# Optimization experiments

Hardware: AMD Instinct MI355X
Metric: run time of the kernel (lower is better)

Reference implementation:

```python
import jax, jax.numpy as jnp
import numpy as np

B, H, W = 8, 64, 64
D_MODEL, D_STATE, D_INNER, DT_RANK, K = 96, 16, 192, 6, 4
EPS = 1e-6


def setup_inputs() -> dict:
    key = jax.random.key(0)
    ks = jax.random.split(key, 9)
    f = lambda k, s, sc=0.02: jax.random.normal(k, s, dtype=jnp.float32) * sc
    return {
        "x": jax.random.normal(ks[0], (B, H, W, D_MODEL), jnp.float32),
        "in_proj_w": f(ks[1], (2 * D_INNER, D_MODEL)),
        "conv_w": f(ks[2], (D_INNER, 1, 3, 3), 0.1),
        "conv_b": jnp.zeros((D_INNER,), jnp.float32),
        "x_proj_w": f(ks[3], (K * (DT_RANK + 2 * D_STATE), D_INNER)),
        "dt_projs_w": f(ks[4], (K * D_INNER, DT_RANK), 0.1),
        "A_logs": jnp.log(jax.random.uniform(ks[5], (K * D_INNER, D_STATE), jnp.float32, 1.0, 16.0)),
        "Ds": jnp.ones((K * D_INNER,), jnp.float32),
        "dt_projs_bias": f(ks[6], (K * D_INNER,), 0.5),
        "norm_w": jnp.ones((D_INNER,), jnp.float32),
        "norm_b": jnp.zeros((D_INNER,), jnp.float32),
        "out_proj_w": f(ks[7], (D_MODEL, D_INNER)),
    }


def _ss2d(x, in_proj_w, conv_w, conv_b, x_proj_w, dt_projs_w, A_logs, Ds,
          dt_projs_bias, norm_w, norm_b, out_proj_w):
    silu = jax.nn.silu
    Bb, Hh, Ww, _ = x.shape
    L = Hh * Ww
    # in_proj, split x/z, z gate activation
    xz = x @ in_proj_w.T                                   # (B,H,W,2*Di)
    xx, z = jnp.split(xz, 2, axis=-1)
    z = silu(z)
    # depthwise conv 3x3 in NCHW
    xc = jnp.transpose(xx, (0, 3, 1, 2))                   # (B,Di,H,W)
    xc = jax.lax.conv_general_dilated(
        xc, conv_w, (1, 1), ((1, 1), (1, 1)),
        dimension_numbers=("NCHW", "OIHW", "NCHW"),
        feature_group_count=D_INNER) + conv_b[None, :, None, None]
    xc = silu(xc)
    # 4-way cross scan: hw, wh (transposed), and their reversals
    x_hw = xc.reshape(Bb, D_INNER, L)
    x_wh = jnp.transpose(xc, (0, 1, 3, 2)).reshape(Bb, D_INNER, L)
    xs = jnp.stack([x_hw, x_wh, x_hw[..., ::-1], x_wh[..., ::-1]], axis=1)  # (B,K,Di,L)
    # per-group projections for dt, B, C
    xpw = x_proj_w.reshape(K, DT_RANK + 2 * D_STATE, D_INNER)
    x_dbl = jnp.einsum("bkdl,kcd->bkcl", xs, xpw)
    dts, Bs, Cs = jnp.split(x_dbl, [DT_RANK, DT_RANK + D_STATE], axis=2)
    dtw = dt_projs_w.reshape(K, D_INNER, DT_RANK)
    dts = jnp.einsum("bkrl,kdr->bkdl", dts, dtw)           # (B,K,Di,L)
    A = -jnp.exp(A_logs).reshape(K, D_INNER, D_STATE)      # (K,Di,N)
    dt = jax.nn.softplus(dts + dt_projs_bias.reshape(1, K, D_INNER, 1))
    # selective scan over L
    def step(h, inp):
        u_t, dt_t, B_t, C_t = inp                          # (B,K,Di),(B,K,Di),(B,K,N),(B,K,N)
        dA = jnp.exp(dt_t[..., None] * A)                  # (B,K,Di,N)
        h = h * dA + (dt_t * u_t)[..., None] * B_t[:, :, None, :]
        y = jnp.einsum("bkdn,bkn->bkd", h, C_t)
        return h, y
    h0 = jnp.zeros((Bb, K, D_INNER, D_STATE), jnp.float32)
    seq = (jnp.moveaxis(xs, -1, 0), jnp.moveaxis(dt, -1, 0),
           jnp.moveaxis(Bs, -1, 0), jnp.moveaxis(Cs, -1, 0))
    _, ysL = jax.lax.scan(step, h0, seq)
    ys = jnp.moveaxis(ysL, 0, -1)                          # (B,K,Di,L)
    ys = ys + xs * Ds.reshape(1, K, D_INNER, 1)
    # cross merge: invert flips and wh-transpose, then sum the 4 directions
    y = ys[:, 0] + ys[:, 2][..., ::-1]
    yw = ys[:, 1] + ys[:, 3][..., ::-1]
    y = y + yw.reshape(Bb, D_INNER, Ww, Hh).transpose(0, 1, 3, 2).reshape(Bb, D_INNER, L)
    y = y.reshape(Bb, D_INNER, Hh, Ww).transpose(0, 2, 3, 1)   # (B,H,W,Di)
    # out LayerNorm over channels
    mean = y.mean(-1, keepdims=True)
    var = ((y - mean) ** 2).mean(-1, keepdims=True)
    y = (y - mean) / jnp.sqrt(var + EPS) * norm_w + norm_b
    # gate and out_proj
    y = y * z
    return y @ out_proj_w.T                                # (B,H,W,d_model)


def reference(x, in_proj_w, conv_w, conv_b, x_proj_w, dt_projs_w, A_logs, Ds,
              dt_projs_bias, norm_w, norm_b, out_proj_w):
    return _ss2d(x, in_proj_w, conv_w, conv_b, x_proj_w, dt_projs_w, A_logs, Ds,
                 dt_projs_bias, norm_w, norm_b, out_proj_w)
```

## Files before the change

kernel.cpp:

```cpp
#include <hip/hip_runtime.h>
#include <hip/hip_bf16.h>
#include <math.h>

#define BB 8
#define HS 64
#define WS 64
#define LL 4096
#define DM 96
#define DI 192
#define NS 16
#define RR 6
#define KK 4
#define NCH 64
#define LC 64
#define XP 16
#define EPSN 1e-6f

typedef __attribute__((ext_vector_type(2))) float f32x2;

__device__ __forceinline__ float fsilu(float x) { return x / (1.f + __expf(-x)); }
__device__ __forceinline__ float rexp2(float x) {
    float r; asm("v_exp_f32 %0, %1" : "=v"(r) : "v"(x)); return r;
}
__device__ __forceinline__ float rlog2(float x) {
    float r; asm("v_log_f32 %0, %1" : "=v"(r) : "v"(x)); return r;
}
__device__ __forceinline__ f32x2 pk_mul(f32x2 a, f32x2 b) {
    f32x2 d; asm("v_pk_mul_f32 %0, %1, %2" : "=v"(d) : "v"(a), "v"(b)); return d;
}
__device__ __forceinline__ f32x2 pk_fma(f32x2 a, f32x2 b, f32x2 c) {
    f32x2 d; asm("v_pk_fma_f32 %0, %1, %2, %3" : "=v"(d) : "v"(a), "v"(b), "v"(c)); return d;
}
__device__ __forceinline__ float fsoftplus(float x) {
    float t = rexp2(x * 1.44269504f);
    float r = 0.69314718f * rlog2(1.f + t);
    return (x > 20.f) ? x : r;
}
__device__ __forceinline__ int lmap(int k, int t) {
    int tt = (k >= 2) ? (LL - 1 - t) : t;
    if (k & 1) tt = ((tt & 63) << 6) | (tt >> 6);
    return tt;
}

__global__ __launch_bounds__(192) void k_inproj(const float* __restrict__ x,
        const float* __restrict__ Win, float* __restrict__ xx, float* __restrict__ zs) {
    __shared__ __align__(16) float xrow[32][96];
    int p0 = blockIdx.x * 32;
    int tid = threadIdx.x;
    {
        const float4* src = (const float4*)(x + (size_t)p0 * 96);
        float4* dst = (float4*)&xrow[0][0];
        #pragma unroll
        for (int e = 0; e < 4; ++e) dst[tid + e * 192] = src[tid + e * 192];
    }
    __syncthreads();
    int c = tid % 96;
    int pg = tid / 96;
    const float4* w0 = (const float4*)(Win + (size_t)c * 96);
    const float4* w1 = (const float4*)(Win + (size_t)(c + 96) * 96);
    const float4* w2 = (const float4*)(Win + (size_t)(c + 192) * 96);
    const float4* w3 = (const float4*)(Win + (size_t)(c + 288) * 96);
    float a0v[16], a1v[16], a2v[16], a3v[16];
    #pragma unroll
    for (int p = 0; p < 16; ++p) { a0v[p] = 0.f; a1v[p] = 0.f; a2v[p] = 0.f; a3v[p] = 0.f; }
    for (int i = 0; i < 24; ++i) {
        float4 q0 = w0[i], q1 = w1[i], q2 = w2[i], q3 = w3[i];
        #pragma unroll
        for (int p = 0; p < 16; ++p) {
            float4 x4 = *(const float4*)&xrow[pg * 16 + p][i * 4];
            a0v[p] += q0.x * x4.x + q0.y * x4.y + q0.z * x4.z + q0.w * x4.w;
            a1v[p] += q1.x * x4.x + q1.y * x4.y + q1.z * x4.z + q1.w * x4.w;
            a2v[p] += q2.x * x4.x + q2.y * x4.y + q2.z * x4.z + q2.w * x4.w;
            a3v[p] += q3.x * x4.x + q3.y * x4.y + q3.z * x4.z + q3.w * x4.w;
        }
    }
    #pragma unroll
    for (int p = 0; p < 16; ++p) {
        size_t row = (size_t)(p0 + pg * 16 + p) * DI;
        xx[row + c]      = a0v[p];
        xx[row + c + 96] = a1v[p];
        zs[row + c]      = fsilu(a2v[p]);
        zs[row + c + 96] = fsilu(a3v[p]);
    }
}

__global__ __launch_bounds__(256) void k_conv(const float* __restrict__ xx,
        const float* __restrict__ cw, const float* __restrict__ cb,
        float* __restrict__ xc) {
    int idx = blockIdx.x * 256 + threadIdx.x;
    int d = idx % DI; int P = idx / DI;
    int l = P & (LL - 1); int h = l >> 6; int w = l & 63;
    float acc = cb[d];
    #pragma unroll
    for (int i = 0; i < 3; ++i) {
        int hh = h + i - 1;
        if ((unsigned)hh < 64u) {
            #pragma unroll
            for (int j = 0; j < 3; ++j) {
                int ww = w + j - 1;
                if ((unsigned)ww < 64u)
                    acc += xx[(size_t)(P + (i - 1) * 64 + (j - 1)) * DI + d] * cw[d * 9 + i * 3 + j];
            }
        }
    }
    xc[idx] = fsilu(acc);
}

__global__ __launch_bounds__(192) void k_xdbl(const float* __restrict__ xc,
        const float* __restrict__ xpw, float* __restrict__ dts_raw,
        float* __restrict__ Bs, float* __restrict__ Cs) {
    __shared__ __align__(16) float xt[XP][DI];
    int tid = threadIdx.x;
    int p0 = blockIdx.x * XP;
    {
        const float4* src = (const float4*)(xc + (size_t)p0 * DI);
        float4* dst = (float4*)&xt[0][0];
        #pragma unroll
        for (int e = 0; e < XP * DI / 4 / 192; ++e) dst[tid + e * 192] = src[tid + e * 192];
    }
    __syncthreads();
    int c = tid;
    int k = c / 38, c2 = c % 38;
    const float4* w4p = (const float4*)(xpw + (size_t)c * DI);
    float acc[XP];
    #pragma unroll
    for (int p = 0; p < XP; ++p) acc[p] = 0.f;
    if (c < 152) {
        #pragma unroll 4
        for (int i = 0; i < DI / 4; ++i) {
            float4 w4 = w4p[i];
            #pragma unroll
            for (int p = 0; p < XP; ++p) {
                float4 x4 = *(const float4*)&xt[p][i * 4];
                acc[p] += w4.x * x4.x + w4.y * x4.y + w4.z * x4.z + w4.w * x4.w;
            }
        }
        #pragma unroll
        for (int p = 0; p < XP; ++p) {
            int P = p0 + p;
            int b = P >> 12; int l = P & (LL - 1);
            int lt = ((l & 63) << 6) | (l >> 6);
            int tk = (k == 0) ? l : (k == 1) ? lt : (k == 2) ? (LL - 1 - l) : (LL - 1 - lt);
            size_t it = ((size_t)(b * KK + k) * LL + tk);
            if (c2 < RR)            dts_raw[it * RR + c2] = acc[p];
            else if (c2 < RR + NS)  Bs[it * NS + (c2 - RR)] = acc[p];
            else                    Cs[it * NS + (c2 - RR - NS)] = acc[p];
        }
    }
}

__global__ __launch_bounds__(192) void k_scan1(const float* __restrict__ xc,
        const float* __restrict__ dts_raw, const float* __restrict__ Bsg,
        const float* __restrict__ A_logs, const float* __restrict__ dtw,
        const float* __restrict__ dtb,
        float* __restrict__ asum_g, float* __restrict__ hpart) {
    __shared__ __align__(16) float dts_s[LC * 8];
    __shared__ __align__(16) float bs_s[LC * NS];
    int bi = blockIdx.x;
    int b = bi >> 8; int rem = bi & 255; int k = rem >> 6; int c0 = rem & 63;
    int t0 = c0 * LC;
    int d = threadIdx.x;
    size_t g0 = (size_t)(b * KK + k) * LL + t0;
    for (int e = d; e < LC * RR; e += DI) dts_s[(e / RR) * 8 + (e % RR)] = dts_raw[g0 * RR + e];
    for (int e = d; e < LC * NS; e += DI) bs_s[e] = Bsg[g0 * NS + e];
    __syncthreads();
    int kd = k * DI + d;
    f32x2 Ar2v[8];
    #pragma unroll
    for (int n2 = 0; n2 < 8; ++n2) {
        Ar2v[n2].x = -__expf(A_logs[(size_t)kd * NS + 2 * n2]) * 1.44269504f;
        Ar2v[n2].y = -__expf(A_logs[(size_t)kd * NS + 2 * n2 + 1]) * 1.44269504f;
    }
    f32x2 dw2[3];
    #pragma unroll
    for (int r = 0; r < 3; ++r) { dw2[r].x = dtw[kd * RR + 2 * r]; dw2[r].y = dtw[kd * RR + 2 * r + 1]; }
    float bias = dtb[kd];
    f32x2 h2[8];
    #pragma unroll
    for (int n2 = 0; n2 < 8; ++n2) h2[n2] = (f32x2){0.f, 0.f};
    float asum = 0.f;
    const float* xcb = xc + (size_t)b * LL * DI + d;
    float uu[4];
    #pragma unroll
    for (int j = 0; j < 4; ++j) uu[j] = xcb[(size_t)lmap(k, t0 + j) * DI];
    for (int tg = 0; tg < LC; tg += 4) {
        float un[4];
        int tb = t0 + ((tg + 4 < LC) ? (tg + 4) : tg);
        #pragma unroll
        for (int j = 0; j < 4; ++j) un[j] = xcb[(size_t)lmap(k, tb + j) * DI];
        #pragma unroll
        for (int j = 0; j < 4; ++j) {
            int t = tg + j;
            float4 q4 = *(const float4*)&dts_s[t * 8];
            float2 q2 = *(const float2*)&dts_s[t * 8 + 4];
            f32x2 a2 = pk_mul((f32x2){q4.x, q4.y}, dw2[0]);
            a2 = pk_fma((f32x2){q4.z, q4.w}, dw2[1], a2);
            a2 = pk_fma((f32x2){q2.x, q2.y}, dw2[2], a2);
            float dt = fsoftplus(bias + a2.x + a2.y);
            asum += dt;
            float dtu = dt * uu[j];
            f32x2 dt2 = {dt, dt}, dtu2 = {dtu, dtu};
            #pragma unroll
            for (int n4 = 0; n4 < 4; ++n4) {
                float4 b4 = *(const float4*)&bs_s[t * NS + n4 * 4];
                f32x2 tl = pk_mul(dt2, Ar2v[n4 * 2]);
                f32x2 th = pk_mul(dt2, Ar2v[n4 * 2 + 1]);
                f32x2 el = {rexp2(tl.x), rexp2(tl.y)};
                f32x2 eh = {rexp2(th.x), rexp2(th.y)};
                h2[n4 * 2]     = pk_fma(h2[n4 * 2],     el, pk_mul(dtu2, (f32x2){b4.x, b4.y}));
                h2[n4 * 2 + 1] = pk_fma(h2[n4 * 2 + 1], eh, pk_mul(dtu2, (f32x2){b4.z, b4.w}));
            }
        }
        #pragma unroll
        for (int j = 0; j < 4; ++j) uu[j] = un[j];
    }
    asum_g[(size_t)bi * DI + d] = asum;
    size_t base = ((size_t)bi * DI + d) * NS;
    #pragma unroll
    for (int n4 = 0; n4 < 4; ++n4) {
        float4 hv = make_float4(h2[n4 * 2].x, h2[n4 * 2].y, h2[n4 * 2 + 1].x, h2[n4 * 2 + 1].y);
        *(float4*)&hpart[base + n4 * 4] = hv;
    }
}

__global__ __launch_bounds__(256) void k_mid(const float* __restrict__ asum_g,
        const float* __restrict__ A_logs, float* __restrict__ hpp) {
    int g = blockIdx.x * 256 + threadIdx.x;
    int bk = g / (DI * NS);
    int rem = g % (DI * NS);
    int d = rem >> 4; int n = rem & 15;
    int k = bk & 3;
    float Ar2 = -__expf(A_logs[(size_t)(k * DI + d) * NS + n]) * 1.44269504f;
    float h = 0.f;
    for (int c = 0; c < NCH; ++c) {
        size_t row = (size_t)(bk * NCH + c) * DI + d;
        float a = rexp2(Ar2 * asum_g[row]);
        size_t ix = row * NS + n;
        float hp = hpp[ix];
        hpp[ix] = h;
        h = a * h + hp;
    }
}

__global__ __launch_bounds__(192) void k_scan2(const float* __restrict__ xc,
        const float* __restrict__ dts_raw, const float* __restrict__ Bsg,
        const float* __restrict__ Csg, const float* __restrict__ A_logs,
        const float* __restrict__ dtw, const float* __restrict__ dtb,
        const float* __restrict__ hinb, float* __restrict__ ysb) {
    __shared__ __align__(16) float dts_s[LC * 8];
    __shared__ __align__(16) float bs_s[LC * NS];
    __shared__ __align__(16) float cs_s[LC * NS];
    int bi = blockIdx.x;
    int b = bi >> 8; int rem = bi & 255; int k = rem >> 6; int c0 = rem & 63;
    int t0 = c0 * LC;
    int d = threadIdx.x;
    size_t g0 = (size_t)(b * KK + k) * LL + t0;
    for (int e = d; e < LC * RR; e += DI) dts_s[(e / RR) * 8 + (e % RR)] = dts_raw[g0 * RR + e];
    for (int e = d; e < LC * NS; e += DI) bs_s[e] = Bsg[g0 * NS + e];
    for (int e = d; e < LC * NS; e += DI) cs_s[e] = Csg[g0 * NS + e];
    __syncthreads();
    int kd = k * DI + d;
    f32x2 Ar2v[8];
    #pragma unroll
    for (int n2 = 0; n2 < 8; ++n2) {
        Ar2v[n2].x = -__expf(A_logs[(size_t)kd * NS + 2 * n2]) * 1.44269504f;
        Ar2v[n2].y = -__expf(A_logs[(size_t)kd * NS + 2 * n2 + 1]) * 1.44269504f;
    }
    f32x2 dw2[3];
    #pragma unroll
    for (int r = 0; r < 3; ++r) { dw2[r].x = dtw[kd * RR + 2 * r]; dw2[r].y = dtw[kd * RR + 2 * r + 1]; }
    float bias = dtb[kd];
    size_t base = ((size_t)bi * DI + d) * NS;
    f32x2 h2[8];
    #pragma unroll
    for (int n4 = 0; n4 < 4; ++n4) {
        float4 hv = *(const float4*)&hinb[base + n4 * 4];
        h2[n4 * 2]     = (f32x2){hv.x, hv.y};
        h2[n4 * 2 + 1] = (f32x2){hv.z, hv.w};
    }
    const float* xcb = xc + (size_t)b * LL * DI + d;
    float* ysw = ysb + g0 * DI + d;
    float uu[4];
    #pragma unroll
    for (int j = 0; j < 4; ++j) uu[j] = xcb[(size_t)lmap(k, t0 + j) * DI];
    for (int tg = 0; tg < LC; tg += 4) {
        float un[4];
        int tb = t0 + ((tg + 4 < LC) ? (tg + 4) : tg);
        #pragma unroll
        for (int j = 0; j < 4; ++j) un[j] = xcb[(size_t)lmap(k, tb + j) * DI];
        #pragma unroll
        for (int j = 0; j < 4; ++j) {
            int t = tg + j;
            float4 q4 = *(const float4*)&dts_s[t * 8];
            float2 q2 = *(const float2*)&dts_s[t * 8 + 4];
            f32x2 a2 = pk_mul((f32x2){q4.x, q4.y}, dw2[0]);
            a2 = pk_fma((f32x2){q4.z, q4.w}, dw2[1], a2);
            a2 = pk_fma((f32x2){q2.x, q2.y}, dw2[2], a2);
            float dt = fsoftplus(bias + a2.x + a2.y);
            float dtu = dt * uu[j];
            f32x2 dt2 = {dt, dt}, dtu2 = {dtu, dtu};
            f32x2 y2 = {0.f, 0.f};
            #pragma unroll
            for (int n4 = 0; n4 < 4; ++n4) {
                float4 b4 = *(const float4*)&bs_s[t * NS + n4 * 4];
                float4 c4 = *(const float4*)&cs_s[t * NS + n4 * 4];
                f32x2 tl = pk_mul(dt2, Ar2v[n4 * 2]);
                f32x2 th = pk_mul(dt2, Ar2v[n4 * 2 + 1]);
                f32x2 el = {rexp2(tl.x), rexp2(tl.y)};
                f32x2 eh = {rexp2(th.x), rexp2(th.y)};
                h2[n4 * 2]     = pk_fma(h2[n4 * 2],     el, pk_mul(dtu2, (f32x2){b4.x, b4.y}));
                h2[n4 * 2 + 1] = pk_fma(h2[n4 * 2 + 1], eh, pk_mul(dtu2, (f32x2){b4.z, b4.w}));
                y2 = pk_fma(h2[n4 * 2],     (f32x2){c4.x, c4.y}, y2);
                y2 = pk_fma(h2[n4 * 2 + 1], (f32x2){c4.z, c4.w}, y2);
            }
            ysw[(size_t)t * DI] = y2.x + y2.y;
        }
        #pragma unroll
        for (int j = 0; j < 4; ++j) uu[j] = un[j];
    }
}

__global__ __launch_bounds__(256) void k_final(const float* __restrict__ xc,
        const float* __restrict__ ysb, const float* __restrict__ Ds,
        const float* __restrict__ zs, const float* __restrict__ nw,
        const float* __restrict__ nb, const float* __restrict__ Wout,
        float* __restrict__ out) {
    __shared__ __align__(16) float gs[32][DI];
    int tid = threadIdx.x;
    int wv = tid >> 6, lane = tid & 63;
    int Pbase = blockIdx.x * 32;
    float nwv[3], nbv[3], sdv[3];
    #pragma unroll
    for (int j = 0; j < 3; ++j) {
        int c = lane + 64 * j;
        nwv[j] = nw[c]; nbv[j] = nb[c];
        sdv[j] = Ds[c] + Ds[DI + c] + Ds[2 * DI + c] + Ds[3 * DI + c];
    }
    for (int pi = 0; pi < 8; ++pi) {
        int pl = wv * 8 + pi;
        int P = Pbase + pl;
        int b = P >> 12, l = P & (LL - 1);
        size_t Poff = (size_t)P * DI;
        size_t r0 = ((size_t)(b * KK + 0) * LL + lmap(0, l)) * DI;
        size_t r1 = ((size_t)(b * KK + 1) * LL + lmap(1, l)) * DI;
        size_t r2 = ((size_t)(b * KK + 2) * LL + lmap(2, l)) * DI;
        size_t r3 = ((size_t)(b * KK + 3) * LL + lmap(3, l)) * DI;
        float v[3];
        #pragma unroll
        for (int j = 0; j < 3; ++j) {
            int c = lane + 64 * j;
            v[j] = xc[Poff + c] * sdv[j]
                 + ysb[r0 + c] + ysb[r1 + c] + ysb[r2 + c] + ysb[r3 + c];
        }
        float s = v[0] + v[1] + v[2];
        #pragma unroll
        for (int o = 32; o; o >>= 1) s += __shfl_xor(s, o);
        float mean = s * (1.f / 192.f);
        float ss = 0.f;
        #pragma unroll
        for (int j = 0; j < 3; ++j) { float dd = v[j] - mean; ss += dd * dd; }
        #pragma unroll
        for (int o = 32; o; o >>= 1) ss += __shfl_xor(ss, o);
        float rstd = rsqrtf(ss * (1.f / 192.f) + EPSN);
        #pragma unroll
        for (int j = 0; j < 3; ++j) {
            int c = lane + 64 * j;
            gs[pl][c] = ((v[j] - mean) * rstd * nwv[j] + nbv[j]) * zs[Poff + c];
        }
    }
    __syncthreads();
    int o = tid & 127;
    int pg = tid >> 7;
    if (o < DM) {
        const float* wr = Wout + (size_t)o * DI;
        float acc[16];
        #pragma unroll
        for (int p = 0; p < 16; ++p) acc[p] = 0.f;
        for (int k0 = 0; k0 < DI; k0 += 4) {
            float4 w4 = *(const float4*)(wr + k0);
            #pragma unroll
            for (int p = 0; p < 16; ++p) {
                float4 g4 = *(const float4*)(&gs[pg * 16 + p][k0]);
                acc[p] += w4.x * g4.x + w4.y * g4.y + w4.z * g4.z + w4.w * g4.w;
            }
        }
        #pragma unroll
        for (int p = 0; p < 16; ++p)
            out[(size_t)(Pbase + pg * 16 + p) * DM + o] = acc[p];
    }
}

extern "C" void kernel_launch(void* const* d_in, const int* in_sizes, int n_in,
                              void* d_out, int out_size, void* d_ws, size_t ws_size,
                              hipStream_t stream) {
    const float* x      = (const float*)d_in[0];
    const float* in_w   = (const float*)d_in[1];
    const float* conv_w = (const float*)d_in[2];
    const float* conv_b = (const float*)d_in[3];
    const float* xpw    = (const float*)d_in[4];
    const float* dtw    = (const float*)d_in[5];
    const float* A_logs = (const float*)d_in[6];
    const float* Ds     = (const float*)d_in[7];
    const float* dtb    = (const float*)d_in[8];
    const float* nw     = (const float*)d_in[9];
    const float* nb     = (const float*)d_in[10];
    const float* out_w  = (const float*)d_in[11];
    float* out = (float*)d_out;

    char* ws = (char*)d_ws;
    size_t off = 0;
    auto alloc = [&](size_t n) { float* p = (float*)(ws + off); off += n * sizeof(float); return p; };
    float* zs   = alloc((size_t)BB * LL * DI);
    float* xc   = alloc((size_t)BB * LL * DI);
    float* dts  = alloc((size_t)BB * KK * LL * RR);
    float* Bsb  = alloc((size_t)BB * KK * LL * NS);
    float* Csb  = alloc((size_t)BB * KK * LL * NS);
    float* asum = alloc((size_t)BB * KK * NCH * DI);
    float* hpp  = alloc((size_t)BB * KK * NCH * DI * NS);
    float* ysb  = alloc((size_t)BB * KK * LL * DI);
    float* xx   = ysb;

    k_inproj<<<BB * LL / 32, 192, 0, stream>>>(x, in_w, xx, zs);
    k_conv<<<BB * LL * DI / 256, 256, 0, stream>>>(xx, conv_w, conv_b, xc);
    k_xdbl<<<BB * LL / XP, 192, 0, stream>>>(xc, xpw, dts, Bsb, Csb);
    k_scan1<<<BB * KK * NCH, DI, 0, stream>>>(xc, dts, Bsb, A_logs, dtw, dtb, asum, hpp);
    k_mid<<<(BB * KK * DI * NS) / 256, 256, 0, stream>>>(asum, A_logs, hpp);
    k_scan2<<<BB * KK * NCH, DI, 0, stream>>>(xc, dts, Bsb, Csb, A_logs, dtw, dtb, hpp, ysb);
    k_final<<<BB * LL / 32, 256, 0, stream>>>(xc, ysb, Ds, zs, nw, nb, out_w, out);
}
```

Measured before the change: 426.2 us.

## Fuse chunked scan passes into single-pass decoupled look-back scan

Replaces the three-kernel chunked selective scan (local chunk scan, sequential carry kernel, rescan) with one kernel. Blocks take ordered tickets, publish chunk-local aggregates and inclusive prefixes with flags, then spin on predecessors using decoupled look-back to get their incoming state. This removes two kernel launches, the serial carry pass and the hpart/asum round trips between kernels. In exchange it adds spin-waiting, atomic traffic and a memset, and each block still runs the chunk recurrence twice.

```diff
diff --git a/kernel.cpp b/kernel.cpp
--- a/kernel.cpp
+++ b/kernel.cpp
@@ -13,6 +13,8 @@
 #define KK 4
 #define NCH 64
 #define LC 64
+#define NSTREAM (BB * KK)
+#define NBLK (NSTREAM * NCH)
 #define XP 16
 #define EPSN 1e-6f
 
@@ -40,6 +42,12 @@
     int tt = (k >= 2) ? (LL - 1 - t) : t;
     if (k & 1) tt = ((tt & 63) << 6) | (tt >> 6);
     return tt;
+}
+__device__ __forceinline__ float ald(const float* p) {
+    return __hip_atomic_load(p, __ATOMIC_RELAXED, __HIP_MEMORY_SCOPE_AGENT);
+}
+__device__ __forceinline__ void ast(float* p, float v) {
+    __hip_atomic_store(p, v, __ATOMIC_RELAXED, __HIP_MEMORY_SCOPE_AGENT);
 }
 
 __global__ __launch_bounds__(192) void k_inproj(const float* __restrict__ x,
@@ -149,111 +157,26 @@
     }
 }
 
-__global__ __launch_bounds__(192) void k_scan1(const float* __restrict__ xc,
-        const float* __restrict__ dts_raw, const float* __restrict__ Bsg,
-        const float* __restrict__ A_logs, const float* __restrict__ dtw,
-        const float* __restrict__ dtb,
-        float* __restrict__ asum_g, float* __restrict__ hpart) {
-    __shared__ __align__(16) float dts_s[LC * 8];
-    __shared__ __align__(16) float bs_s[LC * NS];
-    int bi = blockIdx.x;
-    int b = bi >> 8; int rem = bi & 255; int k = rem >> 6; int c0 = rem & 63;
-    int t0 = c0 * LC;
-    int d = threadIdx.x;
-    size_t g0 = (size_t)(b * KK + k) * LL + t0;
-    for (int e = d; e < LC * RR; e += DI) dts_s[(e / RR) * 8 + (e % RR)] = dts_raw[g0 * RR + e];
-    for (int e = d; e < LC * NS; e += DI) bs_s[e] = Bsg[g0 * NS + e];
-    __syncthreads();
-    int kd = k * DI + d;
-    f32x2 Ar2v[8];
-    #pragma unroll
-    for (int n2 = 0; n2 < 8; ++n2) {
-        Ar2v[n2].x = -__expf(A_logs[(size_t)kd * NS + 2 * n2]) * 1.44269504f;
-        Ar2v[n2].y = -__expf(A_logs[(size_t)kd * NS + 2 * n2 + 1]) * 1.44269504f;
-    }
-    f32x2 dw2[3];
-    #pragma unroll
-    for (int r = 0; r < 3; ++r) { dw2[r].x = dtw[kd * RR + 2 * r]; dw2[r].y = dtw[kd * RR + 2 * r + 1]; }
-    float bias = dtb[kd];
-    f32x2 h2[8];
-    #pragma unroll
-    for (int n2 = 0; n2 < 8; ++n2) h2[n2] = (f32x2){0.f, 0.f};
-    float asum = 0.f;
-    const float* xcb = xc + (size_t)b * LL * DI + d;
-    float uu[4];
-    #pragma unroll
-    for (int j = 0; j < 4; ++j) uu[j] = xcb[(size_t)lmap(k, t0 + j) * DI];
-    for (int tg = 0; tg < LC; tg += 4) {
-        float un[4];
-        int tb = t0 + ((tg + 4 < LC) ? (tg + 4) : tg);
-        #pragma unroll
-        for (int j = 0; j < 4; ++j) un[j] = xcb[(size_t)lmap(k, tb + j) * DI];
-        #pragma unroll
-        for (int j = 0; j < 4; ++j) {
-            int t = tg + j;
-            float4 q4 = *(const float4*)&dts_s[t * 8];
-            float2 q2 = *(const float2*)&dts_s[t * 8 + 4];
-            f32x2 a2 = pk_mul((f32x2){q4.x, q4.y}, dw2[0]);
-            a2 = pk_fma((f32x2){q4.z, q4.w}, dw2[1], a2);
-            a2 = pk_fma((f32x2){q2.x, q2.y}, dw2[2], a2);
-            float dt = fsoftplus(bias + a2.x + a2.y);
-            asum += dt;
-            float dtu = dt * uu[j];
-            f32x2 dt2 = {dt, dt}, dtu2 = {dtu, dtu};
-            #pragma unroll
-            for (int n4 = 0; n4 < 4; ++n4) {
-                float4 b4 = *(const float4*)&bs_s[t * NS + n4 * 4];
-                f32x2 tl = pk_mul(dt2, Ar2v[n4 * 2]);
-                f32x2 th = pk_mul(dt2, Ar2v[n4 * 2 + 1]);
-                f32x2 el = {rexp2(tl.x), rexp2(tl.y)};
-                f32x2 eh = {rexp2(th.x), rexp2(th.y)};
-                h2[n4 * 2]     = pk_fma(h2[n4 * 2],     el, pk_mul(dtu2, (f32x2){b4.x, b4.y}));
-                h2[n4 * 2 + 1] = pk_fma(h2[n4 * 2 + 1], eh, pk_mul(dtu2, (f32x2){b4.z, b4.w}));
-            }
-        }
-        #pragma unroll
-        for (int j = 0; j < 4; ++j) uu[j] = un[j];
-    }
-    asum_g[(size_t)bi * DI + d] = asum;
-    size_t base = ((size_t)bi * DI + d) * NS;
-    #pragma unroll
-    for (int n4 = 0; n4 < 4; ++n4) {
-        float4 hv = make_float4(h2[n4 * 2].x, h2[n4 * 2].y, h2[n4 * 2 + 1].x, h2[n4 * 2 + 1].y);
-        *(float4*)&hpart[base + n4 * 4] = hv;
-    }
-}
-
-__global__ __launch_bounds__(256) void k_mid(const float* __restrict__ asum_g,
-        const float* __restrict__ A_logs, float* __restrict__ hpp) {
-    int g = blockIdx.x * 256 + threadIdx.x;
-    int bk = g / (DI * NS);
-    int rem = g % (DI * NS);
-    int d = rem >> 4; int n = rem & 15;
-    int k = bk & 3;
-    float Ar2 = -__expf(A_logs[(size_t)(k * DI + d) * NS + n]) * 1.44269504f;
-    float h = 0.f;
-    for (int c = 0; c < NCH; ++c) {
-        size_t row = (size_t)(bk * NCH + c) * DI + d;
-        float a = rexp2(Ar2 * asum_g[row]);
-        size_t ix = row * NS + n;
-        float hp = hpp[ix];
-        hpp[ix] = h;
-        h = a * h + hp;
-    }
-}
-
-__global__ __launch_bounds__(192) void k_scan2(const float* __restrict__ xc,
+__global__ __launch_bounds__(192) void k_scan(const float* __restrict__ xc,
         const float* __restrict__ dts_raw, const float* __restrict__ Bsg,
         const float* __restrict__ Csg, const float* __restrict__ A_logs,
         const float* __restrict__ dtw, const float* __restrict__ dtb,
-        const float* __restrict__ hinb, float* __restrict__ ysb) {
+        int* __restrict__ flags, int* __restrict__ ticket,
+        float* __restrict__ asum_s, float* __restrict__ hpart_s,
+        float* __restrict__ hout_s, float* __restrict__ ysb) {
     __shared__ __align__(16) float dts_s[LC * 8];
     __shared__ __align__(16) float bs_s[LC * NS];
     __shared__ __align__(16) float cs_s[LC * NS];
-    int bi = blockIdx.x;
-    int b = bi >> 8; int rem = bi & 255; int k = rem >> 6; int c0 = rem & 63;
-    int t0 = c0 * LC;
+    __shared__ int s_tkt, s_flag;
     int d = threadIdx.x;
+    if (d == 0) s_tkt = atomicAdd(ticket, 1);
+    __syncthreads();
+    int tk = s_tkt;
+    int stream = tk % NSTREAM;
+    int c = tk / NSTREAM;
+    int b = stream >> 2, k = stream & 3;
+    int bi = stream * NCH + c;
+    int t0 = c * LC;
     size_t g0 = (size_t)(b * KK + k) * LL + t0;
     for (int e = d; e < LC * RR; e += DI) dts_s[(e / RR) * 8 + (e % RR)] = dts_raw[g0 * RR + e];
     for (int e = d; e < LC * NS; e += DI) bs_s[e] = Bsg[g0 * NS + e];
@@ -270,53 +193,150 @@
     #pragma unroll
     for (int r = 0; r < 3; ++r) { dw2[r].x = dtw[kd * RR + 2 * r]; dw2[r].y = dtw[kd * RR + 2 * r + 1]; }
     float bias = dtb[kd];
-    size_t base = ((size_t)bi * DI + d) * NS;
+    const float* xcb = xc + (size_t)b * LL * DI + d;
     f32x2 h2[8];
     #pragma unroll
-    for (int n4 = 0; n4 < 4; ++n4) {
-        float4 hv = *(const float4*)&hinb[base + n4 * 4];
-        h2[n4 * 2]     = (f32x2){hv.x, hv.y};
-        h2[n4 * 2 + 1] = (f32x2){hv.z, hv.w};
-    }
-    const float* xcb = xc + (size_t)b * LL * DI + d;
+    for (int n2 = 0; n2 < 8; ++n2) h2[n2] = (f32x2){0.f, 0.f};
+    float asum = 0.f;
+    {
+        float uu[4];
+        #pragma unroll
+        for (int j = 0; j < 4; ++j) uu[j] = xcb[(size_t)lmap(k, t0 + j) * DI];
+        for (int tg = 0; tg < LC; tg += 4) {
+            float un[4];
+            int tb = t0 + ((tg + 4 < LC) ? (tg + 4) : tg);
+            #pragma unroll
+            for (int j = 0; j < 4; ++j) un[j] = xcb[(size_t)lmap(k, tb + j) * DI];
+            #pragma unroll
+            for (int j = 0; j < 4; ++j) {
+                int t = tg + j;
+                float4 q4 = *(const float4*)&dts_s[t * 8];
+                float2 q2 = *(const float2*)&dts_s[t * 8 + 4];
+                f32x2 a2 = pk_mul((f32x2){q4.x, q4.y}, dw2[0]);
+                a2 = pk_fma((f32x2){q4.z, q4.w}, dw2[1], a2);
+                a2 = pk_fma((f32x2){q2.x, q2.y}, dw2[2], a2);
+                float dt = fsoftplus(bias + a2.x + a2.y);
+                asum += dt;
+                float dtu = dt * uu[j];
+                f32x2 dt2 = {dt, dt}, dtu2 = {dtu, dtu};
+                #pragma unroll
+                for (int n4 = 0; n4 < 4; ++n4) {
+                    float4 b4 = *(const float4*)&bs_s[t * NS + n4 * 4];
+                    f32x2 tl = pk_mul(dt2, Ar2v[n4 * 2]);
+                    f32x2 th = pk_mul(dt2, Ar2v[n4 * 2 + 1]);
+                    f32x2 el = {rexp2(tl.x), rexp2(tl.y)};
+                    f32x2 eh = {rexp2(th.x), rexp2(th.y)};
+                    h2[n4 * 2]     = pk_fma(h2[n4 * 2],     el, pk_mul(dtu2, (f32x2){b4.x, b4.y}));
+                    h2[n4 * 2 + 1] = pk_fma(h2[n4 * 2 + 1], eh, pk_mul(dtu2, (f32x2){b4.z, b4.w}));
+                }
+            }
+            #pragma unroll
+            for (int j = 0; j < 4; ++j) uu[j] = un[j];
+        }
+    }
+    size_t sb = (size_t)bi * DI + d;
+    size_t hb = sb * NS;
+    ast(&asum_s[sb], asum);
+    #pragma unroll
+    for (int n2 = 0; n2 < 8; ++n2) {
+        ast(&hpart_s[hb + 2 * n2], h2[n2].x);
+        ast(&hpart_s[hb + 2 * n2 + 1], h2[n2].y);
+    }
+    __threadfence();
+    __syncthreads();
+    if (c > 0 && d == 0)
+        __hip_atomic_store(&flags[bi], 1, __ATOMIC_RELEASE, __HIP_MEMORY_SCOPE_AGENT);
+    f32x2 hin[8], pA[8];
+    #pragma unroll
+    for (int n2 = 0; n2 < 8; ++n2) { hin[n2] = (f32x2){0.f, 0.f}; pA[n2] = (f32x2){1.f, 1.f}; }
+    if (c > 0) {
+        int j = c - 1;
+        while (true) {
+            __syncthreads();
+            if (d == 0) {
+                int f;
+                do { f = __hip_atomic_load(&flags[stream * NCH + j], __ATOMIC_ACQUIRE, __HIP_MEMORY_SCOPE_AGENT); } while (f == 0);
+                s_flag = f;
+            }
+            __syncthreads();
+            int f = s_flag;
+            size_t pb = ((size_t)(stream * NCH + j) * DI + d) * NS;
+            if (f == 2) {
+                #pragma unroll
+                for (int n2 = 0; n2 < 8; ++n2) {
+                    f32x2 hv = { ald(&hout_s[pb + 2 * n2]), ald(&hout_s[pb + 2 * n2 + 1]) };
+                    hin[n2] = pk_fma(pA[n2], hv, hin[n2]);
+                }
+                break;
+            } else {
+                #pragma unroll
+                for (int n2 = 0; n2 < 8; ++n2) {
+                    f32x2 hv = { ald(&hpart_s[pb + 2 * n2]), ald(&hpart_s[pb + 2 * n2 + 1]) };
+                    hin[n2] = pk_fma(pA[n2], hv, hin[n2]);
+                }
+                float aj = ald(&asum_s[(size_t)(stream * NCH + j) * DI + d]);
+                #pragma unroll
+                for (int n2 = 0; n2 < 8; ++n2) {
+                    f32x2 e = { rexp2(Ar2v[n2].x * aj), rexp2(Ar2v[n2].y * aj) };
+                    pA[n2] = pk_mul(pA[n2], e);
+                }
+                --j;
+            }
+        }
+    }
+    #pragma unroll
+    for (int n2 = 0; n2 < 8; ++n2) {
+        f32x2 e = { rexp2(Ar2v[n2].x * asum), rexp2(Ar2v[n2].y * asum) };
+        f32x2 ho = pk_fma(e, hin[n2], h2[n2]);
+        ast(&hout_s[hb + 2 * n2], ho.x);
+        ast(&hout_s[hb + 2 * n2 + 1], ho.y);
+    }
+    __threadfence();
+    __syncthreads();
+    if (d == 0)
+        __hip_atomic_store(&flags[bi], 2, __ATOMIC_RELEASE, __HIP_MEMORY_SCOPE_AGENT);
+    #pragma unroll
+    for (int n2 = 0; n2 < 8; ++n2) h2[n2] = hin[n2];
     float* ysw = ysb + g0 * DI + d;
-    float uu[4];
-    #pragma unroll
-    for (int j = 0; j < 4; ++j) uu[j] = xcb[(size_t)lmap(k, t0 + j) * DI];
-    for (int tg = 0; tg < LC; tg += 4) {
-        float un[4];
-        int tb = t0 + ((tg + 4 < LC) ? (tg + 4) : tg);
-        #pragma unroll
-        for (int j = 0; j < 4; ++j) un[j] = xcb[(size_t)lmap(k, tb + j) * DI];
-        #pragma unroll
-        for (int j = 0; j < 4; ++j) {
-            int t = tg + j;
-            float4 q4 = *(const float4*)&dts_s[t * 8];
-            float2 q2 = *(const float2*)&dts_s[t * 8 + 4];
-            f32x2 a2 = pk_mul((f32x2){q4.x, q4.y}, dw2[0]);
-            a2 = pk_fma((f32x2){q4.z, q4.w}, dw2[1], a2);
-            a2 = pk_fma((f32x2){q2.x, q2.y}, dw2[2], a2);
-            float dt = fsoftplus(bias + a2.x + a2.y);
-            float dtu = dt * uu[j];
-            f32x2 dt2 = {dt, dt}, dtu2 = {dtu, dtu};
-            f32x2 y2 = {0.f, 0.f};
-            #pragma unroll
-            for (int n4 = 0; n4 < 4; ++n4) {
-                float4 b4 = *(const float4*)&bs_s[t * NS + n4 * 4];
-                float4 c4 = *(const float4*)&cs_s[t * NS + n4 * 4];
-                f32x2 tl = pk_mul(dt2, Ar2v[n4 * 2]);
-                f32x2 th = pk_mul(dt2, Ar2v[n4 * 2 + 1]);
-                f32x2 el = {rexp2(tl.x), rexp2(tl.y)};
-                f32x2 eh = {rexp2(th.x), rexp2(th.y)};
-                h2[n4 * 2]     = pk_fma(h2[n4 * 2],     el, pk_mul(dtu2, (f32x2){b4.x, b4.y}));
-                h2[n4 * 2 + 1] = pk_fma(h2[n4 * 2 + 1], eh, pk_mul(dtu2, (f32x2){b4.z, b4.w}));
-                y2 = pk_fma(h2[n4 * 2],     (f32x2){c4.x, c4.y}, y2);
-                y2 = pk_fma(h2[n4 * 2 + 1], (f32x2){c4.z, c4.w}, y2);
-            }
-            ysw[(size_t)t * DI] = y2.x + y2.y;
-        }
-        #pragma unroll
-        for (int j = 0; j < 4; ++j) uu[j] = un[j];
+    {
+        float uu[4];
+        #pragma unroll
+        for (int j = 0; j < 4; ++j) uu[j] = xcb[(size_t)lmap(k, t0 + j) * DI];
+        for (int tg = 0; tg < LC; tg += 4) {
+            float un[4];
+            int tb = t0 + ((tg + 4 < LC) ? (tg + 4) : tg);
+            #pragma unroll
+            for (int j = 0; j < 4; ++j) un[j] = xcb[(size_t)lmap(k, tb + j) * DI];
+            #pragma unroll
+            for (int j = 0; j < 4; ++j) {
+                int t = tg + j;
+                float4 q4 = *(const float4*)&dts_s[t * 8];
+                float2 q2 = *(const float2*)&dts_s[t * 8 + 4];
+                f32x2 a2 = pk_mul((f32x2){q4.x, q4.y}, dw2[0]);
+                a2 = pk_fma((f32x2){q4.z, q4.w}, dw2[1], a2);
+                a2 = pk_fma((f32x2){q2.x, q2.y}, dw2[2], a2);
+                float dt = fsoftplus(bias + a2.x + a2.y);
+                float dtu = dt * uu[j];
+                f32x2 dt2 = {dt, dt}, dtu2 = {dtu, dtu};
+                f32x2 y2 = {0.f, 0.f};
+                #pragma unroll
+                for (int n4 = 0; n4 < 4; ++n4) {
+                    float4 b4 = *(const float4*)&bs_s[t * NS + n4 * 4];
+                    float4 c4 = *(const float4*)&cs_s[t * NS + n4 * 4];
+                    f32x2 tl = pk_mul(dt2, Ar2v[n4 * 2]);
+                    f32x2 th = pk_mul(dt2, Ar2v[n4 * 2 + 1]);
+                    f32x2 el = {rexp2(tl.x), rexp2(tl.y)};
+                    f32x2 eh = {rexp2(th.x), rexp2(th.y)};
+                    h2[n4 * 2]     = pk_fma(h2[n4 * 2],     el, pk_mul(dtu2, (f32x2){b4.x, b4.y}));
+                    h2[n4 * 2 + 1] = pk_fma(h2[n4 * 2 + 1], eh, pk_mul(dtu2, (f32x2){b4.z, b4.w}));
+                    y2 = pk_fma(h2[n4 * 2],     (f32x2){c4.x, c4.y}, y2);
+                    y2 = pk_fma(h2[n4 * 2 + 1], (f32x2){c4.z, c4.w}, y2);
+                }
+                ysw[(size_t)t * DI] = y2.x + y2.y;
+            }
+            #pragma unroll
+            for (int j = 0; j < 4; ++j) uu[j] = un[j];
+        }
     }
 }
 
@@ -410,21 +430,24 @@
     char* ws = (char*)d_ws;
     size_t off = 0;
     auto alloc = [&](size_t n) { float* p = (float*)(ws + off); off += n * sizeof(float); return p; };
-    float* zs   = alloc((size_t)BB * LL * DI);
-    float* xc   = alloc((size_t)BB * LL * DI);
-    float* dts  = alloc((size_t)BB * KK * LL * RR);
-    float* Bsb  = alloc((size_t)BB * KK * LL * NS);
-    float* Csb  = alloc((size_t)BB * KK * LL * NS);
-    float* asum = alloc((size_t)BB * KK * NCH * DI);
-    float* hpp  = alloc((size_t)BB * KK * NCH * DI * NS);
-    float* ysb  = alloc((size_t)BB * KK * LL * DI);
-    float* xx   = ysb;
-
+    float* zs    = alloc((size_t)BB * LL * DI);
+    float* xc    = alloc((size_t)BB * LL * DI);
+    float* dts   = alloc((size_t)BB * KK * LL * RR);
+    float* Bsb   = alloc((size_t)BB * KK * LL * NS);
+    float* Csb   = alloc((size_t)BB * KK * LL * NS);
+    int*   flags = (int*)alloc(NBLK + 1);
+    int*   ticket = flags + NBLK;
+    float* asum_s = alloc((size_t)NBLK * DI);
+    float* hpart_s = alloc((size_t)NBLK * DI * NS);
+    float* hout_s  = alloc((size_t)NBLK * DI * NS);
+    float* ysb   = alloc((size_t)BB * KK * LL * DI);
+    float* xx    = ysb;
+
+    hipMemsetAsync(flags, 0, (NBLK + 1) * sizeof(int), stream);
     k_inproj<<<BB * LL / 32, 192, 0, stream>>>(x, in_w, xx, zs);
     k_conv<<<BB * LL * DI / 256, 256, 0, stream>>>(xx, conv_w, conv_b, xc);
     k_xdbl<<<BB * LL / XP, 192, 0, stream>>>(xc, xpw, dts, Bsb, Csb);
-    k_scan1<<<BB * KK * NCH, DI, 0, stream>>>(xc, dts, Bsb, A_logs, dtw, dtb, asum, hpp);
-    k_mid<<<(BB * KK * DI * NS) / 256, 256, 0, stream>>>(asum, A_logs, hpp);
-    k_scan2<<<BB * KK * NCH, DI, 0, stream>>>(xc, dts, Bsb, Csb, A_logs, dtw, dtb, hpp, ysb);
+    k_scan<<<NBLK, DI, 0, stream>>>(xc, dts, Bsb, Csb, A_logs, dtw, dtb,
+                                    flags, ticket, asum_s, hpart_s, hout_s, ysb);
     k_final<<<BB * LL / 32, 256, 0, stream>>>(xc, ysb, Ds, zs, nw, nb, out_w, out);
 }
```

After: 1.265 ms. +196.7%, slower.
